# Kernel optimization log

Hardware: AMD Instinct MI355X
Metric: run time of the kernel (lower is better)

Reference implementation:

```python
import jax, jax.numpy as jnp
import numpy as np

C_POS_W = 1.0
C_NEG_W = 0.5
MARGIN = 0.0
LOGIT_SCALE = 100.0
EPS = 1e-06


def setup_inputs() -> dict:
    key = jax.random.key(0)
    N = 8192
    sim_matrix = jax.random.normal(key, (N, N), dtype=jnp.float32)
    return {"sim_matrix": sim_matrix}


def reference(sim_matrix) -> jnp.ndarray:
    N = sim_matrix.shape[0]
    # row softmax with logit scale, clamped like the torch module
    logpt = jax.nn.softmax(sim_matrix * LOGIT_SCALE, axis=-1)
    logpt = jnp.clip(logpt, EPS, 1.0 - EPS)

    pos = jnp.diagonal(logpt)            # [N] positive probabilities
    d = jnp.diagonal(sim_matrix)         # [N] positive similarities

    # double relu margin: violation vs row-positive and column-positive
    max_margin = (jax.nn.relu(MARGIN + sim_matrix - d[:, None])
                  + jax.nn.relu(MARGIN + sim_matrix - d[None, :]))
    eye = jnp.eye(N, dtype=bool)
    max_margin = jnp.where(eye, 0.0, max_margin)

    sel = max_margin > 0.0               # hard-negative selection mask
    cnt = jnp.sum(sel)

    loss_pos = -jnp.log(pos)             # [N]
    neg_terms = -jnp.log(1.0 - logpt)    # [N, N]
    neg_sum = jnp.sum(jnp.where(sel, neg_terms, 0.0))
    loss_neg_mean = neg_sum / jnp.maximum(cnt, 1).astype(neg_sum.dtype)

    sim_loss = C_POS_W * jnp.mean(loss_pos) + jnp.where(
        cnt > 0, C_NEG_W * loss_neg_mean, jnp.zeros((), dtype=loss_pos.dtype))
    return sim_loss
```

## Files before the change

### kernel.cpp

```cpp
#include <hip/hip_runtime.h>
#include <math.h>

namespace {

constexpr int N   = 8192;
constexpr int NT  = 256;
constexpr int PF4 = N / 4 / NT;
constexpr int NW  = NT / 64;
constexpr float EPS = 1e-6f;
constexpr float NLOG_EPS = 13.815511f;
constexpr float NEG_INF  = -3.4e38f;

__device__ __forceinline__ float waveMax(float v) {
#pragma unroll
  for (int off = 32; off; off >>= 1) v = fmaxf(v, __shfl_xor(v, off, 64));
  return v;
}
__device__ __forceinline__ float waveSum(float v) {
#pragma unroll
  for (int off = 32; off; off >>= 1) v += __shfl_xor(v, off, 64);
  return v;
}
__device__ __forceinline__ unsigned waveSumU(unsigned v) {
#pragma unroll
  for (int off = 32; off; off >>= 1) v += (unsigned)__shfl_xor((int)v, off, 64);
  return v;
}

__global__ void diag_extract(const float* __restrict__ sim, float* __restrict__ dg) {
  int i = blockIdx.x * blockDim.x + threadIdx.x;
  if (i < N) dg[i] = sim[(size_t)i * N + i];
}

__launch_bounds__(NT)
__global__ void row_loss(const float* __restrict__ sim,
                         const float* __restrict__ dg,
                         float* __restrict__ pos_out,
                         float* __restrict__ neg_out,
                         unsigned* __restrict__ cnt_out) {
  __shared__ float shm[NW];
  __shared__ float shz[NW];
  __shared__ float shn[NW];
  __shared__ float shp[NW];
  __shared__ unsigned shc[NW];

  const int row  = blockIdx.x;
  const int t    = threadIdx.x;
  const int wid  = t >> 6;
  const int lane = t & 63;

  const float4* rp = reinterpret_cast<const float4*>(sim + (size_t)row * N);
  const float4* dp = reinterpret_cast<const float4*>(dg);
  const float dr = dg[row];

  float t1 = NEG_INF, t2 = NEG_INF;
  float s1 = NEG_INF, s2 = NEG_INF;
  unsigned lc = 0;

#pragma unroll
  for (int k = 0; k < PF4; ++k) {
    float4 v  = rp[k * NT + t];
    float4 dv = dp[k * NT + t];
#pragma unroll
    for (int c = 0; c < 4; ++c) {
      const float xi = (c == 0) ? v.x  : (c == 1) ? v.y  : (c == 2) ? v.z  : v.w;
      const float dc = (c == 0) ? dv.x : (c == 1) ? dv.y : (c == 2) ? dv.z : dv.w;
      const bool sel = xi > fminf(dr, dc);
      lc += sel ? 1u : 0u;
      t2 = fmaxf(t2, fminf(xi, t1));
      t1 = fmaxf(t1, xi);
      const float xs = sel ? xi : NEG_INF;
      s2 = fmaxf(s2, fminf(xs, s1));
      s1 = fmaxf(s1, xs);
    }
  }

  float lm = waveMax(t1);
  if (lane == 0) shm[wid] = lm;
  __syncthreads();
  float M = shm[0];
#pragma unroll
  for (int w = 1; w < NW; ++w) M = fmaxf(M, shm[w]);

  const float zc = M - 0.2f;
  float zp = 0.0f;
  if (t1 > zc) zp += __expf(100.0f * (t1 - M));
  if (t2 > zc) zp += __expf(100.0f * (t2 - M));
  zp = waveSum(zp);
  if (lane == 0) shz[wid] = zp;
  __syncthreads();
  float Z = shz[0];
#pragma unroll
  for (int w = 1; w < NW; ++w) Z += shz[w];

  const float C    = fmaf(100.0f, M, __logf(Z));
  const float xthr = (C - NLOG_EPS) * 0.01f;

  float posv = 0.0f;
  if (t == 0) {
    float pd = __expf(fmaf(100.0f, dr, -C));
    pd = fminf(fmaxf(pd, EPS), 1.0f - EPS);
    posv = -__logf(pd);
  }

  float negs = 0.0f;
  if (s1 > xthr) {
    float p  = __expf(fmaf(100.0f, s1, -C));
    float pc = fminf(fmaxf(p, EPS), 1.0f - EPS);
    negs += -__logf(1.0f - pc) - EPS;
  }
  if (s2 > xthr) {
    float p  = __expf(fmaf(100.0f, s2, -C));
    float pc = fminf(fmaxf(p, EPS), 1.0f - EPS);
    negs += -__logf(1.0f - pc) - EPS;
  }
  negs += EPS * (float)lc;

  negs = waveSum(negs);
  posv = waveSum(posv);
  lc   = waveSumU(lc);
  if (lane == 0) { shn[wid] = negs; shp[wid] = posv; shc[wid] = lc; }
  __syncthreads();
  if (t == 0) {
    float bp = 0.0f, bn = 0.0f;
    unsigned bc = 0;
#pragma unroll
    for (int w = 0; w < NW; ++w) { bp += shp[w]; bn += shn[w]; bc += shc[w]; }
    pos_out[row] = bp;
    neg_out[row] = bn;
    cnt_out[row] = bc;
  }
}

__launch_bounds__(1024)
__global__ void reduce_final(const float* __restrict__ pos_in,
                             const float* __restrict__ neg_in,
                             const unsigned* __restrict__ cnt_in,
                             float* __restrict__ out) {
  __shared__ double shp[16], shn[16];
  __shared__ unsigned long long shc[16];

  const int t    = threadIdx.x;
  const int wid  = t >> 6;
  const int lane = t & 63;

  float ps = 0.0f, ns = 0.0f;
  unsigned cs = 0;
  const float4* pp = reinterpret_cast<const float4*>(pos_in);
  const float4* np = reinterpret_cast<const float4*>(neg_in);
  const uint4*  cp = reinterpret_cast<const uint4*>(cnt_in);
#pragma unroll
  for (int k = 0; k < 2; ++k) {
    float4 a = pp[k * 1024 + t];
    float4 b = np[k * 1024 + t];
    uint4  c = cp[k * 1024 + t];
    ps += a.x + a.y + a.z + a.w;
    ns += b.x + b.y + b.z + b.w;
    cs += c.x + c.y + c.z + c.w;
  }
  ps = waveSum(ps);
  ns = waveSum(ns);
  cs = waveSumU(cs);
  if (lane == 0) { shp[wid] = (double)ps; shn[wid] = (double)ns; shc[wid] = (unsigned long long)cs; }
  __syncthreads();
  if (t == 0) {
    double bp = 0.0, bn = 0.0;
    unsigned long long bc = 0;
#pragma unroll
    for (int w = 0; w < 16; ++w) { bp += shp[w]; bn += shn[w]; bc += shc[w]; }
    double pos_mean = bp / (double)N;
    double neg = (bc > 0ull) ? 0.5 * (bn / (double)bc) : 0.0;
    out[0] = (float)(pos_mean + neg);
  }
}

}

extern "C" void kernel_launch(void* const* d_in, const int* in_sizes, int n_in,
                              void* d_out, int out_size, void* d_ws, size_t ws_size,
                              hipStream_t stream) {
  const float* sim = (const float*)d_in[0];
  float* out = (float*)d_out;

  float*    pos = (float*)d_ws;
  float*    neg = (float*)((char*)d_ws + 32 * 1024);
  unsigned* cnt = (unsigned*)((char*)d_ws + 64 * 1024);
  float*    dg  = (float*)((char*)d_ws + 96 * 1024);

  diag_extract<<<N / 256, 256, 0, stream>>>(sim, dg);
  row_loss<<<N, NT, 0, stream>>>(sim, dg, pos, neg, cnt);
  reduce_final<<<1, 1024, 0, stream>>>(pos, neg, cnt, out);
}
```

Baseline: 58.36 us.

## Process four rows per block to reuse diagonal loads and amortize reductions

Each block now handles four consecutive rows, loading each diagonal float4 once and reusing it across those rows. The block-level reductions and barriers are shared across the four rows, and the grid shrinks by a factor of four. The aim is less diagonal traffic and lower per-block overhead. In exchange, register pressure rises, fewer blocks are available to hide memory latency, and there are more loads in flight per thread.

```diff
diff --git a/kernel.cpp b/kernel.cpp
--- a/kernel.cpp
+++ b/kernel.cpp
@@ -5,6 +5,7 @@
 
 constexpr int N   = 8192;
 constexpr int NT  = 256;
+constexpr int TR  = 4;
 constexpr int PF4 = N / 4 / NT;
 constexpr int NW  = NT / 64;
 constexpr float EPS = 1e-6f;
@@ -38,97 +39,124 @@
                          float* __restrict__ pos_out,
                          float* __restrict__ neg_out,
                          unsigned* __restrict__ cnt_out) {
-  __shared__ float shm[NW];
-  __shared__ float shz[NW];
-  __shared__ float shn[NW];
-  __shared__ float shp[NW];
-  __shared__ unsigned shc[NW];
-
-  const int row  = blockIdx.x;
+  __shared__ float shm[TR][NW];
+  __shared__ float shz[TR][NW];
+  __shared__ float shn[TR][NW];
+  __shared__ unsigned shc[TR][NW];
+
+  const int row0 = blockIdx.x * TR;
   const int t    = threadIdx.x;
   const int wid  = t >> 6;
   const int lane = t & 63;
 
-  const float4* rp = reinterpret_cast<const float4*>(sim + (size_t)row * N);
   const float4* dp = reinterpret_cast<const float4*>(dg);
-  const float dr = dg[row];
-
-  float t1 = NEG_INF, t2 = NEG_INF;
-  float s1 = NEG_INF, s2 = NEG_INF;
-  unsigned lc = 0;
+
+  float dr[TR];
+#pragma unroll
+  for (int r = 0; r < TR; ++r) dr[r] = dg[row0 + r];
+
+  float t1[TR], t2[TR], s1[TR], s2[TR];
+  unsigned lc[TR];
+#pragma unroll
+  for (int r = 0; r < TR; ++r) {
+    t1[r] = NEG_INF; t2[r] = NEG_INF;
+    s1[r] = NEG_INF; s2[r] = NEG_INF;
+    lc[r] = 0;
+  }
 
 #pragma unroll
   for (int k = 0; k < PF4; ++k) {
-    float4 v  = rp[k * NT + t];
-    float4 dv = dp[k * NT + t];
-#pragma unroll
-    for (int c = 0; c < 4; ++c) {
-      const float xi = (c == 0) ? v.x  : (c == 1) ? v.y  : (c == 2) ? v.z  : v.w;
-      const float dc = (c == 0) ? dv.x : (c == 1) ? dv.y : (c == 2) ? dv.z : dv.w;
-      const bool sel = xi > fminf(dr, dc);
-      lc += sel ? 1u : 0u;
-      t2 = fmaxf(t2, fminf(xi, t1));
-      t1 = fmaxf(t1, xi);
-      const float xs = sel ? xi : NEG_INF;
-      s2 = fmaxf(s2, fminf(xs, s1));
-      s1 = fmaxf(s1, xs);
-    }
-  }
-
-  float lm = waveMax(t1);
-  if (lane == 0) shm[wid] = lm;
-  __syncthreads();
-  float M = shm[0];
-#pragma unroll
-  for (int w = 1; w < NW; ++w) M = fmaxf(M, shm[w]);
-
-  const float zc = M - 0.2f;
-  float zp = 0.0f;
-  if (t1 > zc) zp += __expf(100.0f * (t1 - M));
-  if (t2 > zc) zp += __expf(100.0f * (t2 - M));
-  zp = waveSum(zp);
-  if (lane == 0) shz[wid] = zp;
-  __syncthreads();
-  float Z = shz[0];
-#pragma unroll
-  for (int w = 1; w < NW; ++w) Z += shz[w];
-
-  const float C    = fmaf(100.0f, M, __logf(Z));
-  const float xthr = (C - NLOG_EPS) * 0.01f;
-
-  float posv = 0.0f;
+    const int idx = k * NT + t;
+    float4 dv = dp[idx];
+#pragma unroll
+    for (int r = 0; r < TR; ++r) {
+      const float4* rp = reinterpret_cast<const float4*>(sim + (size_t)(row0 + r) * N);
+      float4 v = rp[idx];
+#pragma unroll
+      for (int c = 0; c < 4; ++c) {
+        const float xi = (c == 0) ? v.x  : (c == 1) ? v.y  : (c == 2) ? v.z  : v.w;
+        const float dc = (c == 0) ? dv.x : (c == 1) ? dv.y : (c == 2) ? dv.z : dv.w;
+        const bool sel = xi > fminf(dr[r], dc);
+        lc[r] += sel ? 1u : 0u;
+        t2[r] = fmaxf(t2[r], fminf(xi, t1[r]));
+        t1[r] = fmaxf(t1[r], xi);
+        const float xs = sel ? xi : NEG_INF;
+        s2[r] = fmaxf(s2[r], fminf(xs, s1[r]));
+        s1[r] = fmaxf(s1[r], xs);
+      }
+    }
+  }
+
+#pragma unroll
+  for (int r = 0; r < TR; ++r) {
+    float lm = waveMax(t1[r]);
+    if (lane == 0) shm[r][wid] = lm;
+  }
+  __syncthreads();
+
+  float M[TR];
+#pragma unroll
+  for (int r = 0; r < TR; ++r) {
+    float m = shm[r][0];
+#pragma unroll
+    for (int w = 1; w < NW; ++w) m = fmaxf(m, shm[r][w]);
+    M[r] = m;
+  }
+
+#pragma unroll
+  for (int r = 0; r < TR; ++r) {
+    const float zc = M[r] - 0.2f;
+    float zp = 0.0f;
+    if (t1[r] > zc) zp += __expf(100.0f * (t1[r] - M[r]));
+    if (t2[r] > zc) zp += __expf(100.0f * (t2[r] - M[r]));
+    zp = waveSum(zp);
+    if (lane == 0) shz[r][wid] = zp;
+  }
+  __syncthreads();
+
+  float C[TR], xthr[TR];
+#pragma unroll
+  for (int r = 0; r < TR; ++r) {
+    float Z = shz[r][0];
+#pragma unroll
+    for (int w = 1; w < NW; ++w) Z += shz[r][w];
+    C[r]    = fmaf(100.0f, M[r], __logf(Z));
+    xthr[r] = (C[r] - NLOG_EPS) * 0.01f;
+  }
+
+#pragma unroll
+  for (int r = 0; r < TR; ++r) {
+    float negs = 0.0f;
+    if (s1[r] > xthr[r]) {
+      float p  = __expf(fmaf(100.0f, s1[r], -C[r]));
+      float pc = fminf(fmaxf(p, EPS), 1.0f - EPS);
+      negs += -__logf(1.0f - pc) - EPS;
+    }
+    if (s2[r] > xthr[r]) {
+      float p  = __expf(fmaf(100.0f, s2[r], -C[r]));
+      float pc = fminf(fmaxf(p, EPS), 1.0f - EPS);
+      negs += -__logf(1.0f - pc) - EPS;
+    }
+    negs += EPS * (float)lc[r];
+    negs = waveSum(negs);
+    unsigned c = waveSumU(lc[r]);
+    if (lane == 0) { shn[r][wid] = negs; shc[r][wid] = c; }
+  }
+  __syncthreads();
+
   if (t == 0) {
-    float pd = __expf(fmaf(100.0f, dr, -C));
-    pd = fminf(fmaxf(pd, EPS), 1.0f - EPS);
-    posv = -__logf(pd);
-  }
-
-  float negs = 0.0f;
-  if (s1 > xthr) {
-    float p  = __expf(fmaf(100.0f, s1, -C));
-    float pc = fminf(fmaxf(p, EPS), 1.0f - EPS);
-    negs += -__logf(1.0f - pc) - EPS;
-  }
-  if (s2 > xthr) {
-    float p  = __expf(fmaf(100.0f, s2, -C));
-    float pc = fminf(fmaxf(p, EPS), 1.0f - EPS);
-    negs += -__logf(1.0f - pc) - EPS;
-  }
-  negs += EPS * (float)lc;
-
-  negs = waveSum(negs);
-  posv = waveSum(posv);
-  lc   = waveSumU(lc);
-  if (lane == 0) { shn[wid] = negs; shp[wid] = posv; shc[wid] = lc; }
-  __syncthreads();
-  if (t == 0) {
-    float bp = 0.0f, bn = 0.0f;
-    unsigned bc = 0;
-#pragma unroll
-    for (int w = 0; w < NW; ++w) { bp += shp[w]; bn += shn[w]; bc += shc[w]; }
-    pos_out[row] = bp;
-    neg_out[row] = bn;
-    cnt_out[row] = bc;
+#pragma unroll
+    for (int r = 0; r < TR; ++r) {
+      float bn = shn[r][0];
+      unsigned bc = shc[r][0];
+#pragma unroll
+      for (int w = 1; w < NW; ++w) { bn += shn[r][w]; bc += shc[r][w]; }
+      float pd = __expf(fmaf(100.0f, dr[r], -C[r]));
+      pd = fminf(fmaxf(pd, EPS), 1.0f - EPS);
+      pos_out[row0 + r] = -__logf(pd);
+      neg_out[row0 + r] = bn;
+      cnt_out[row0 + r] = bc;
+    }
   }
 }
 
@@ -188,6 +216,6 @@
   float*    dg  = (float*)((char*)d_ws + 96 * 1024);
 
   diag_extract<<<N / 256, 256, 0, stream>>>(sim, dg);
-  row_loss<<<N, NT, 0, stream>>>(sim, dg, pos, neg, cnt);
+  row_loss<<<N / TR, NT, 0, stream>>>(sim, dg, pos, neg, cnt);
   reduce_final<<<1, 1024, 0, stream>>>(pos, neg, cnt, out);
 }
```

After: 97.23 us. 66.6% more time.
